# Kernel optimization log

Measured on AMD Instinct MI355X. Metric: run time of the kernel, lower is better.

Reference implementation:

```python
import jax, jax.numpy as jnp
import numpy as np

B, Q, K, D, H = 4, 512, 2048, 256, 64
NEG = -1000000.0


def setup_inputs() -> dict:
    key = jax.random.key(0)
    ks = jax.random.split(key, 7)
    return {
        "queries": jax.random.normal(ks[0], (B, Q, D), dtype=jnp.float32),
        "keys": jax.random.normal(ks[1], (B, K, D), dtype=jnp.float32),
        "values": jax.random.normal(ks[2], (B, K, D), dtype=jnp.float32),
        "valid_lens": jax.random.randint(ks[3], (B,), 0, K).astype(jnp.int64),
        "Wq": jax.random.normal(ks[4], (D, H), dtype=jnp.float32) * 0.05,
        "Wk": jax.random.normal(ks[5], (D, H), dtype=jnp.float32) * 0.05,
        "wv": jax.random.normal(ks[6], (H,), dtype=jnp.float32) * 0.05,
    }


def reference(queries, keys, values, valid_lens, Wq, Wk, wv):
    # project queries/keys to hidden dim
    q = jnp.einsum("bqd,dh->bqh", queries, Wq)  # (B,Q,H)
    k = jnp.einsum("bkd,dh->bkh", keys, Wk)     # (B,K,H)
    # broadcast add + tanh -> (B,Q,K,H), then reduce to scalar score
    features = jnp.tanh(q[:, :, None, :] + k[:, None, :, :])
    scores = jnp.einsum("bqkh,h->bqk", features, wv)  # (B,Q,K)
    # masked softmax over key axis: positions >= valid_len get -1e6
    mask = jnp.arange(scores.shape[-1]) < valid_lens[:, None, None]  # (B,1,K)
    scores = jnp.where(mask, scores, NEG)
    attn = jax.nn.softmax(scores, axis=-1)
    return jnp.einsum("bqk,bkv->bqv", attn, values)
```

## Files before the change

kernel.cpp:

```cpp
#include <hip/hip_runtime.h>
#include <hip/hip_bf16.h>

#define NB 4
#define NQ 512
#define NK 2048
#define ND 256
#define NH 64
#define QT 8
#define KSPLIT 4

#define SCALE_C 2.8853900817779268f
#define L2E     1.4426950408889634f

__device__ __forceinline__ unsigned short f2b(float f) {
    unsigned u = __float_as_uint(f);
    u += 0x7fffu + ((u >> 16) & 1u);
    return (unsigned short)(u >> 16);
}
__device__ __forceinline__ float b2f_lo(unsigned u) { return __uint_as_float(u << 16); }
__device__ __forceinline__ float b2f_hi(unsigned u) { return __uint_as_float(u & 0xffff0000u); }

__device__ __forceinline__ float wred_sum(float v) {
#pragma unroll
    for (int off = 32; off; off >>= 1) v += __shfl_xor(v, off, 64);
    return v;
}

__global__ __launch_bounds__(256) void proj_kernel(
    const float* __restrict__ queries, const float* __restrict__ keys,
    const float* __restrict__ Wq, const float* __restrict__ Wk,
    float* __restrict__ eq, float4* __restrict__ ek4)
{
    __shared__ __align__(16) float in_lds[16][256];
    const int t = threadIdx.x;
    const int row0 = blockIdx.x * 16;
    const bool isQ = row0 < NB * NQ;
    const float* src = isQ ? (queries + (size_t)row0 * ND)
                           : (keys + (size_t)(row0 - NB * NQ) * ND);
    const float* W = isQ ? Wq : Wk;

    const float4* src4 = (const float4*)src;
#pragma unroll
    for (int i = 0; i < 4; ++i) {
        int f4 = t + 256 * i;
        ((float4*)&in_lds[0][0])[f4] = src4[f4];
    }
    __syncthreads();

    const int w = t >> 6, h = t & 63;
    const int r0 = w * 4;
    float a[4] = {0.f, 0.f, 0.f, 0.f};
#pragma unroll 4
    for (int d4 = 0; d4 < 64; ++d4) {
        const float* Wp = W + (size_t)(d4 * 4) * NH + h;
        float w0 = Wp[0], w1 = Wp[NH], w2 = Wp[2 * NH], w3 = Wp[3 * NH];
#pragma unroll
        for (int i = 0; i < 4; ++i) {
            float4 x = ((const float4*)in_lds[r0 + i])[d4];
            a[i] = fmaf(x.x, w0, fmaf(x.y, w1, fmaf(x.z, w2, fmaf(x.w, w3, a[i]))));
        }
    }
    if (isQ) {
#pragma unroll
        for (int i = 0; i < 4; ++i)
            eq[(size_t)(row0 + r0 + i) * NH + h] =
                __builtin_amdgcn_exp2f(a[i] * SCALE_C);
    } else {
        __syncthreads();
        float* out2 = &in_lds[0][0];
#pragma unroll
        for (int i = 0; i < 4; ++i)
            out2[(r0 + i) * 64 + h] = __builtin_amdgcn_exp2f(a[i] * SCALE_C);
        __syncthreads();
        const int row = t >> 4, hb = t & 15;
        float4 v = *(const float4*)&out2[row * 64 + hb * 4];
        int kr = row0 - NB * NQ + row;
        int b = kr >> 11, k = kr & (NK - 1);
        ek4[((size_t)(b * 16 + hb)) * NK + k] = v;
    }
}

__global__ __launch_bounds__(512, 8) void attn_part(
    const float* __restrict__ values, const int* __restrict__ valid_lens,
    const float* __restrict__ wv,
    const float* __restrict__ eq, const float4* __restrict__ ek4,
    float* __restrict__ po, float* __restrict__ pml)
{
    __shared__ __align__(16) float qp_l[QT][NH];
    __shared__ __align__(16) float wv2_l[NH];
    __shared__ float sumwv_l;
    __shared__ __align__(16) float buf[8192];
    __shared__ float red_l[QT][8];

    unsigned short* p_l = (unsigned short*)buf;

    const int t = threadIdx.x;
    const int n = blockIdx.x;
    const int g = n & 255;
    const int sp = n >> 8;
    const int b  = ((g >> 6) + sp) & 3;
    const int qt = g & 63;
    const int q0 = qt * QT;
    const int wid = t >> 6;
    const int dl = (t & 63) * 4;

    if (t < 128) {
        int q = t >> 4, h4 = t & 15;
        ((float4*)qp_l[q])[h4] =
            ((const float4*)(eq + (size_t)(b * NQ + q0 + q) * NH))[h4];
    }
    if (t < 64) {
        float wvv = wv[t];
        wv2_l[t] = -2.0f * wvv;
        float s = wred_sum(wvv);
        if (t == 0) sumwv_l = s;
    }
    int vl = valid_lens[b];
    const int kv = vl < 0 ? 0 : (vl > NK ? NK : vl);
    const int kveff = (kv == 0) ? NK : kv;
    const int step   = ((kveff + 31) & ~31) >> 2;
    const int kvr8   = (kveff + 7) & ~7;
    const int kstart = sp * step;
    int kend = kstart + step; if (kend > kvr8) kend = kvr8;
    const int range8 = (kend > kstart) ? (kend - kstart) : 0;
    __syncthreads();
    const float sumwv = sumwv_l;

    {
        const int kl = t;
        float sum_q[QT];
#pragma unroll
        for (int q = 0; q < QT; ++q) sum_q[q] = 0.f;
        if (kl < range8) {
            const int kg = kstart + kl;
            float e[QT];
            if (kv == 0) {
#pragma unroll
                for (int q = 0; q < QT; ++q) e[q] = 1.0f;
            } else if (kg < kv) {
                float s[QT];
#pragma unroll
                for (int q = 0; q < QT; ++q) s[q] = sumwv;
                const float4* kT4 = ek4 + (size_t)(b * 16) * NK + kg;
#pragma unroll
                for (int gq = 0; gq < 4; ++gq) {
                    float4 kb[4];
#pragma unroll
                    for (int i = 0; i < 4; ++i)
                        kb[i] = kT4[(size_t)(gq * 4 + i) * NK];
#pragma unroll
                    for (int i = 0; i < 4; ++i) {
                        const int h4 = gq * 4 + i;
                        float4 w4 = ((const float4*)wv2_l)[h4];
                        float4 kh = kb[i];
#pragma unroll
                        for (int q = 0; q < QT; ++q) {
                            float4 qh = ((const float4*)qp_l[q])[h4];
                            float d0 = fmaf(qh.x, kh.x, 1.0f);
                            float d1 = fmaf(qh.y, kh.y, 1.0f);
                            float d2 = fmaf(qh.z, kh.z, 1.0f);
                            float d3 = fmaf(qh.w, kh.w, 1.0f);
                            float d01 = d0 * d1;
                            float d23 = d2 * d3;
                            float n01 = w4.x * d1;
                            n01 = fmaf(w4.y, d0, n01);
                            float n23 = w4.z * d3;
                            n23 = fmaf(w4.w, d2, n23);
                            float num = n01 * d23;
                            num = fmaf(n23, d01, num);
                            float r = __builtin_amdgcn_rcpf(d01 * d23);
                            s[q] = fmaf(num, r, s[q]);
                        }
                    }
                }
#pragma unroll
                for (int q = 0; q < QT; ++q) e[q] = __builtin_amdgcn_exp2f(s[q] * L2E);
            } else {
#pragma unroll
                for (int q = 0; q < QT; ++q) e[q] = 0.f;
            }
            unsigned eb[QT];
#pragma unroll
            for (int q = 0; q < QT; ++q) {
                eb[q] = (unsigned)f2b(e[q]);
                sum_q[q] = b2f_lo(eb[q]);
            }
            uint4 u;
            u.x = eb[0] | (eb[1] << 16);
            u.y = eb[2] | (eb[3] << 16);
            u.z = eb[4] | (eb[5] << 16);
            u.w = eb[6] | (eb[7] << 16);
            *(uint4*)&p_l[(size_t)kl * 8] = u;
        }
#pragma unroll
        for (int q = 0; q < QT; ++q) {
            float s = wred_sum(sum_q[q]);
            if ((t & 63) == 0) red_l[q][wid] = s;
        }
    }
    __syncthreads();

    float4 acc[QT];
#pragma unroll
    for (int q = 0; q < QT; ++q) acc[q] = make_float4(0.f, 0.f, 0.f, 0.f);

    const float* Vb = values + ((size_t)b * NK + kstart) * ND;
#pragma unroll 2
    for (int kl = wid; kl < range8; kl += 8) {
        uint4 u = *(const uint4*)&p_l[(size_t)kl * 8];
        float pr0 = b2f_lo(u.x), pr1 = b2f_hi(u.x);
        float pr2 = b2f_lo(u.y), pr3 = b2f_hi(u.y);
        float pr4 = b2f_lo(u.z), pr5 = b2f_hi(u.z);
        float pr6 = b2f_lo(u.w), pr7 = b2f_hi(u.w);
        float4 v = *(const float4*)(Vb + (size_t)kl * ND + dl);
        acc[0].x = fmaf(pr0, v.x, acc[0].x); acc[0].y = fmaf(pr0, v.y, acc[0].y);
        acc[0].z = fmaf(pr0, v.z, acc[0].z); acc[0].w = fmaf(pr0, v.w, acc[0].w);
        acc[1].x = fmaf(pr1, v.x, acc[1].x); acc[1].y = fmaf(pr1, v.y, acc[1].y);
        acc[1].z = fmaf(pr1, v.z, acc[1].z); acc[1].w = fmaf(pr1, v.w, acc[1].w);
        acc[2].x = fmaf(pr2, v.x, acc[2].x); acc[2].y = fmaf(pr2, v.y, acc[2].y);
        acc[2].z = fmaf(pr2, v.z, acc[2].z); acc[2].w = fmaf(pr2, v.w, acc[2].w);
        acc[3].x = fmaf(pr3, v.x, acc[3].x); acc[3].y = fmaf(pr3, v.y, acc[3].y);
        acc[3].z = fmaf(pr3, v.z, acc[3].z); acc[3].w = fmaf(pr3, v.w, acc[3].w);
        acc[4].x = fmaf(pr4, v.x, acc[4].x); acc[4].y = fmaf(pr4, v.y, acc[4].y);
        acc[4].z = fmaf(pr4, v.z, acc[4].z); acc[4].w = fmaf(pr4, v.w, acc[4].w);
        acc[5].x = fmaf(pr5, v.x, acc[5].x); acc[5].y = fmaf(pr5, v.y, acc[5].y);
        acc[5].z = fmaf(pr5, v.z, acc[5].z); acc[5].w = fmaf(pr5, v.w, acc[5].w);
        acc[6].x = fmaf(pr6, v.x, acc[6].x); acc[6].y = fmaf(pr6, v.y, acc[6].y);
        acc[6].z = fmaf(pr6, v.z, acc[6].z); acc[6].w = fmaf(pr6, v.w, acc[6].w);
        acc[7].x = fmaf(pr7, v.x, acc[7].x); acc[7].y = fmaf(pr7, v.y, acc[7].y);
        acc[7].z = fmaf(pr7, v.z, acc[7].z); acc[7].w = fmaf(pr7, v.w, acc[7].w);
    }
    __syncthreads();

    if (wid >= 4) {
        float* s = buf + (size_t)(wid - 4) * 2048;
#pragma unroll
        for (int q = 0; q < QT; ++q) *(float4*)(s + q * 256 + dl) = acc[q];
    }
    __syncthreads();
    if (wid < 4) {
        const float* s = buf + (size_t)wid * 2048;
#pragma unroll
        for (int q = 0; q < QT; ++q) {
            float4 r = *(const float4*)(s + q * 256 + dl);
            acc[q].x += r.x; acc[q].y += r.y; acc[q].z += r.z; acc[q].w += r.w;
        }
    }
    __syncthreads();
    if (wid >= 2 && wid < 4) {
        float* s = buf + (size_t)(wid - 2) * 2048;
#pragma unroll
        for (int q = 0; q < QT; ++q) *(float4*)(s + q * 256 + dl) = acc[q];
    }
    __syncthreads();
    if (wid < 2) {
        const float* s = buf + (size_t)wid * 2048;
#pragma unroll
        for (int q = 0; q < QT; ++q) {
            float4 r = *(const float4*)(s + q * 256 + dl);
            acc[q].x += r.x; acc[q].y += r.y; acc[q].z += r.z; acc[q].w += r.w;
        }
    }
    __syncthreads();
    if (wid == 1) {
#pragma unroll
        for (int q = 0; q < QT; ++q) *(float4*)(buf + q * 256 + dl) = acc[q];
    }
    __syncthreads();
    if (wid == 0) {
#pragma unroll
        for (int q = 0; q < QT; ++q) {
            float4 r = *(const float4*)(buf + q * 256 + dl);
            acc[q].x += r.x; acc[q].y += r.y; acc[q].z += r.z; acc[q].w += r.w;
            const size_t row4 = ((size_t)(b * NQ + q0 + q) * KSPLIT + sp);
            *(float4*)(po + row4 * ND + dl) = acc[q];
        }
        if (t < QT) {
            float l = 0.f;
#pragma unroll
            for (int i = 0; i < 8; ++i) l += red_l[t][i];
            pml[((size_t)(b * NQ + q0 + t) * KSPLIT + sp)] = l;
        }
    }
}

__global__ __launch_bounds__(256) void combine_kernel(
    const float* __restrict__ po, const float* __restrict__ pml,
    float* __restrict__ out)
{
    const int t = threadIdx.x;
    const int row = blockIdx.x * 4 + (t >> 6);
    const int dl = (t & 63) * 4;
    float l = 0.f;
#pragma unroll
    for (int s = 0; s < KSPLIT; ++s) l += pml[row * KSPLIT + s];
    float4 o = make_float4(0.f, 0.f, 0.f, 0.f);
#pragma unroll
    for (int s = 0; s < KSPLIT; ++s) {
        float4 p = *(const float4*)(po + ((size_t)row * KSPLIT + s) * ND + dl);
        o.x += p.x; o.y += p.y; o.z += p.z; o.w += p.w;
    }
    const float inv = 1.0f / l;
    o.x *= inv; o.y *= inv; o.z *= inv; o.w *= inv;
    *(float4*)(out + (size_t)row * ND + dl) = o;
}

extern "C" void kernel_launch(void* const* d_in, const int* in_sizes, int n_in,
                              void* d_out, int out_size, void* d_ws, size_t ws_size,
                              hipStream_t stream) {
    const float* queries   = (const float*)d_in[0];
    const float* keys      = (const float*)d_in[1];
    const float* values    = (const float*)d_in[2];
    const int* valid_lens  = (const int*)d_in[3];
    const float* Wq        = (const float*)d_in[4];
    const float* Wk        = (const float*)d_in[5];
    const float* wv        = (const float*)d_in[6];
    float* out = (float*)d_out;

    float* eq   = (float*)d_ws;
    float4* ek4 = (float4*)(eq + (size_t)NB * NQ * NH);
    float* po   = (float*)(ek4 + (size_t)NB * 16 * NK);
    float* pml  = po + (size_t)NB * NQ * KSPLIT * ND;

    proj_kernel<<<(NB * NQ + NB * NK) / 16, 256, 0, stream>>>(queries, keys, Wq, Wk, eq, ek4);
    attn_part<<<NB * (NQ / QT) * KSPLIT, 512, 0, stream>>>(values, valid_lens, wv, eq, ek4, po, pml);
    combine_kernel<<<NB * NQ / 4, 256, 0, stream>>>(po, pml, out);
}
```

Before: 58.32 us.

## Balance key work across batches with concatenated valid ranges and atomic accumulation

Instead of splitting each batch's valid key range into four fixed chunks, the kernel concatenates the valid key ranges of all batches and splits the total into 16 equal slices per query tile. This evens out work when valid lengths differ across batches. Partial outputs and softmax denominators are accumulated with float atomics into a buffer that the projection kernel now zeroes. The combine step shrinks to a single normalize, at the cost of atomic traffic, extra per-batch tree reductions within a block, and non-deterministic summation order.

```diff
diff --git a/kernel.cpp b/kernel.cpp
--- a/kernel.cpp
+++ b/kernel.cpp
@@ -7,10 +7,13 @@
 #define ND 256
 #define NH 64
 #define QT 8
-#define KSPLIT 4
+#define NSLICE 16
 
 #define SCALE_C 2.8853900817779268f
 #define L2E     1.4426950408889634f
+
+#define PO_FLOATS ((size_t)NB * NQ * ND)
+#define ACC_FLOATS (PO_FLOATS + (size_t)NB * NQ)
 
 __device__ __forceinline__ unsigned short f2b(float f) {
     unsigned u = __float_as_uint(f);
@@ -29,12 +32,23 @@
 __global__ __launch_bounds__(256) void proj_kernel(
     const float* __restrict__ queries, const float* __restrict__ keys,
     const float* __restrict__ Wq, const float* __restrict__ Wk,
-    float* __restrict__ eq, float4* __restrict__ ek4)
+    float* __restrict__ eq, float4* __restrict__ ek4, float* __restrict__ po_acc)
 {
     __shared__ __align__(16) float in_lds[16][256];
     const int t = threadIdx.x;
     const int row0 = blockIdx.x * 16;
     const bool isQ = row0 < NB * NQ;
+
+    {
+        const size_t zb = (size_t)blockIdx.x * 824;
+#pragma unroll
+        for (int i = 0; i < 4; ++i) {
+            int loc = t + i * 256;
+            size_t idx = zb + loc;
+            if (loc < 824 && idx < ACC_FLOATS) po_acc[idx] = 0.f;
+        }
+    }
+
     const float* src = isQ ? (queries + (size_t)row0 * ND)
                            : (keys + (size_t)(row0 - NB * NQ) * ND);
     const float* W = isQ ? Wq : Wk;
@@ -84,105 +98,106 @@
     const float* __restrict__ values, const int* __restrict__ valid_lens,
     const float* __restrict__ wv,
     const float* __restrict__ eq, const float4* __restrict__ ek4,
-    float* __restrict__ po, float* __restrict__ pml)
+    float* __restrict__ po_acc, float* __restrict__ l_acc)
 {
-    __shared__ __align__(16) float qp_l[QT][NH];
-    __shared__ __align__(16) float wv2_l[NH];
-    __shared__ float sumwv_l;
-    __shared__ __align__(16) float buf[8192];
-    __shared__ float red_l[QT][8];
-
-    unsigned short* p_l = (unsigned short*)buf;
+    __shared__ __align__(16) float smem[6468];
+    unsigned short* p_l = (unsigned short*)smem;
+    float* qp_l  = smem + 2048;
+    float* tree  = smem + 2048;
+    float* red_l = smem + 6144;
+    float* wv2_l = smem + 6400;
 
     const int t = threadIdx.x;
-    const int n = blockIdx.x;
-    const int g = n & 255;
-    const int sp = n >> 8;
-    const int b  = ((g >> 6) + sp) & 3;
-    const int qt = g & 63;
+    const int qt = blockIdx.x & 63;
+    const int sp = blockIdx.x >> 6;
     const int q0 = qt * QT;
     const int wid = t >> 6;
     const int dl = (t & 63) * 4;
 
-    if (t < 128) {
-        int q = t >> 4, h4 = t & 15;
-        ((float4*)qp_l[q])[h4] =
+    {
+        int b = t >> 7, q = (t >> 4) & 7, h4 = t & 15;
+        ((float4*)(qp_l + (size_t)(b * 8 + q) * 64))[h4] =
             ((const float4*)(eq + (size_t)(b * NQ + q0 + q) * NH))[h4];
     }
     if (t < 64) {
         float wvv = wv[t];
         wv2_l[t] = -2.0f * wvv;
         float s = wred_sum(wvv);
-        if (t == 0) sumwv_l = s;
-    }
-    int vl = valid_lens[b];
-    const int kv = vl < 0 ? 0 : (vl > NK ? NK : vl);
-    const int kveff = (kv == 0) ? NK : kv;
-    const int step   = ((kveff + 31) & ~31) >> 2;
-    const int kvr8   = (kveff + 7) & ~7;
-    const int kstart = sp * step;
-    int kend = kstart + step; if (kend > kvr8) kend = kvr8;
-    const int range8 = (kend > kstart) ? (kend - kstart) : 0;
+        if (t == 0) smem[6464] = s;
+    }
+    if (t >= 64 && t < 320) red_l[t - 64] = 0.f;
+
+    int kvb[4], C[5];
+    C[0] = 0;
+#pragma unroll
+    for (int b = 0; b < 4; ++b) {
+        int v = valid_lens[b];
+        v = v < 0 ? 0 : (v > NK ? NK : v);
+        kvb[b] = v;
+        int kveff = (v == 0) ? NK : v;
+        C[b + 1] = C[b] + ((kveff + 7) & ~7);
+    }
+    const int T_all = C[4];
+    const int step = ((T_all + 127) & ~127) >> 4;
+    const int cstart = sp * step;
+    int cend = cstart + step; if (cend > T_all) cend = T_all;
     __syncthreads();
-    const float sumwv = sumwv_l;
+    const float sumwv = smem[6464];
 
     {
-        const int kl = t;
+        const int j = cstart + t;
+        const bool act = j < cend;
+        int bb = 3;
+        if (act) bb = (j >= C[1]) + (j >= C[2]) + (j >= C[3]);
+        const int kg = act ? (j - C[bb]) : 0;
+        const int kvB = kvb[bb];
         float sum_q[QT];
 #pragma unroll
         for (int q = 0; q < QT; ++q) sum_q[q] = 0.f;
-        if (kl < range8) {
-            const int kg = kstart + kl;
-            float e[QT];
-            if (kv == 0) {
-#pragma unroll
-                for (int q = 0; q < QT; ++q) e[q] = 1.0f;
-            } else if (kg < kv) {
-                float s[QT];
-#pragma unroll
-                for (int q = 0; q < QT; ++q) s[q] = sumwv;
-                const float4* kT4 = ek4 + (size_t)(b * 16) * NK + kg;
-#pragma unroll
-                for (int gq = 0; gq < 4; ++gq) {
-                    float4 kb[4];
-#pragma unroll
-                    for (int i = 0; i < 4; ++i)
-                        kb[i] = kT4[(size_t)(gq * 4 + i) * NK];
-#pragma unroll
-                    for (int i = 0; i < 4; ++i) {
-                        const int h4 = gq * 4 + i;
-                        float4 w4 = ((const float4*)wv2_l)[h4];
-                        float4 kh = kb[i];
-#pragma unroll
-                        for (int q = 0; q < QT; ++q) {
-                            float4 qh = ((const float4*)qp_l[q])[h4];
-                            float d0 = fmaf(qh.x, kh.x, 1.0f);
-                            float d1 = fmaf(qh.y, kh.y, 1.0f);
-                            float d2 = fmaf(qh.z, kh.z, 1.0f);
-                            float d3 = fmaf(qh.w, kh.w, 1.0f);
-                            float d01 = d0 * d1;
-                            float d23 = d2 * d3;
-                            float n01 = w4.x * d1;
-                            n01 = fmaf(w4.y, d0, n01);
-                            float n23 = w4.z * d3;
-                            n23 = fmaf(w4.w, d2, n23);
-                            float num = n01 * d23;
-                            num = fmaf(n23, d01, num);
-                            float r = __builtin_amdgcn_rcpf(d01 * d23);
-                            s[q] = fmaf(num, r, s[q]);
-                        }
+        if (act) {
+            float s[QT];
+#pragma unroll
+            for (int q = 0; q < QT; ++q) s[q] = sumwv;
+            const float4* kT4 = ek4 + (size_t)(bb * 16) * NK + kg;
+            const float* qb = qp_l + (size_t)bb * 512;
+#pragma unroll
+            for (int gq = 0; gq < 4; ++gq) {
+                float4 kb[4];
+#pragma unroll
+                for (int i = 0; i < 4; ++i) kb[i] = kT4[(size_t)(gq * 4 + i) * NK];
+#pragma unroll
+                for (int i = 0; i < 4; ++i) {
+                    const int h4 = gq * 4 + i;
+                    float4 w4 = ((const float4*)wv2_l)[h4];
+                    float4 kh = kb[i];
+#pragma unroll
+                    for (int q = 0; q < QT; ++q) {
+                        float4 qh = ((const float4*)(qb + q * 64))[h4];
+                        float d0 = fmaf(qh.x, kh.x, 1.0f);
+                        float d1 = fmaf(qh.y, kh.y, 1.0f);
+                        float d2 = fmaf(qh.z, kh.z, 1.0f);
+                        float d3 = fmaf(qh.w, kh.w, 1.0f);
+                        float d01 = d0 * d1;
+                        float d23 = d2 * d3;
+                        float n01 = w4.x * d1;
+                        n01 = fmaf(w4.y, d0, n01);
+                        float n23 = w4.z * d3;
+                        n23 = fmaf(w4.w, d2, n23);
+                        float num = n01 * d23;
+                        num = fmaf(n23, d01, num);
+                        float r = __builtin_amdgcn_rcpf(d01 * d23);
+                        s[q] = fmaf(num, r, s[q]);
                     }
                 }
-#pragma unroll
-                for (int q = 0; q < QT; ++q) e[q] = __builtin_amdgcn_exp2f(s[q] * L2E);
-            } else {
-#pragma unroll
-                for (int q = 0; q < QT; ++q) e[q] = 0.f;
-            }
+            }
+            const bool valid = kg < kvB;
+            const float fill = (kvB == 0) ? 1.0f : 0.0f;
             unsigned eb[QT];
 #pragma unroll
             for (int q = 0; q < QT; ++q) {
-                eb[q] = (unsigned)f2b(e[q]);
+                float ee = __builtin_amdgcn_exp2f(s[q] * L2E);
+                float ev = valid ? ee : fill;
+                eb[q] = (unsigned)f2b(ev);
                 sum_q[q] = b2f_lo(eb[q]);
             }
             uint4 u;
@@ -190,118 +205,139 @@
             u.y = eb[2] | (eb[3] << 16);
             u.z = eb[4] | (eb[5] << 16);
             u.w = eb[6] | (eb[7] << 16);
-            *(uint4*)&p_l[(size_t)kl * 8] = u;
-        }
-#pragma unroll
-        for (int q = 0; q < QT; ++q) {
-            float s = wred_sum(sum_q[q]);
-            if ((t & 63) == 0) red_l[q][wid] = s;
+            *(uint4*)&p_l[(size_t)t * 8] = u;
+        }
+        const int bb0 = __builtin_amdgcn_readfirstlane(bb);
+        const bool uni = __all(bb == bb0);
+        if (uni) {
+#pragma unroll
+            for (int q = 0; q < QT; ++q) {
+                float s = wred_sum(sum_q[q]);
+                if ((t & 63) == 0) red_l[bb0 * 64 + q * 8 + wid] = s;
+            }
+        } else {
+#pragma unroll 1
+            for (int b2 = 0; b2 < 4; ++b2) {
+#pragma unroll
+                for (int q = 0; q < QT; ++q) {
+                    float s = wred_sum(bb == b2 ? sum_q[q] : 0.f);
+                    if ((t & 63) == 0 && s != 0.f) red_l[b2 * 64 + q * 8 + wid] = s;
+                }
+            }
         }
     }
     __syncthreads();
+    if (t < 32) {
+        int b2 = t >> 3, q = t & 7;
+        float l = 0.f;
+#pragma unroll
+        for (int i = 0; i < 8; ++i) l += red_l[b2 * 64 + q * 8 + i];
+        if (l > 0.f) atomicAdd(&l_acc[b2 * NQ + q0 + q], l);
+    }
 
     float4 acc[QT];
-#pragma unroll
-    for (int q = 0; q < QT; ++q) acc[q] = make_float4(0.f, 0.f, 0.f, 0.f);
-
-    const float* Vb = values + ((size_t)b * NK + kstart) * ND;
+#pragma unroll 1
+    for (int b2 = 0; b2 < 4; ++b2) {
+        int g0 = C[b2] > cstart ? C[b2] : cstart;
+        int g1 = C[b2 + 1] < cend ? C[b2 + 1] : cend;
+        if (g0 >= g1) continue;
+        const int s0 = g0 - cstart, s1 = g1 - cstart;
+        const int kg0 = g0 - C[b2];
+#pragma unroll
+        for (int q = 0; q < QT; ++q) acc[q] = make_float4(0.f, 0.f, 0.f, 0.f);
+        const float* Vb = values + ((size_t)b2 * NK + kg0) * ND;
 #pragma unroll 2
-    for (int kl = wid; kl < range8; kl += 8) {
-        uint4 u = *(const uint4*)&p_l[(size_t)kl * 8];
-        float pr0 = b2f_lo(u.x), pr1 = b2f_hi(u.x);
-        float pr2 = b2f_lo(u.y), pr3 = b2f_hi(u.y);
-        float pr4 = b2f_lo(u.z), pr5 = b2f_hi(u.z);
-        float pr6 = b2f_lo(u.w), pr7 = b2f_hi(u.w);
-        float4 v = *(const float4*)(Vb + (size_t)kl * ND + dl);
-        acc[0].x = fmaf(pr0, v.x, acc[0].x); acc[0].y = fmaf(pr0, v.y, acc[0].y);
-        acc[0].z = fmaf(pr0, v.z, acc[0].z); acc[0].w = fmaf(pr0, v.w, acc[0].w);
-        acc[1].x = fmaf(pr1, v.x, acc[1].x); acc[1].y = fmaf(pr1, v.y, acc[1].y);
-        acc[1].z = fmaf(pr1, v.z, acc[1].z); acc[1].w = fmaf(pr1, v.w, acc[1].w);
-        acc[2].x = fmaf(pr2, v.x, acc[2].x); acc[2].y = fmaf(pr2, v.y, acc[2].y);
-        acc[2].z = fmaf(pr2, v.z, acc[2].z); acc[2].w = fmaf(pr2, v.w, acc[2].w);
-        acc[3].x = fmaf(pr3, v.x, acc[3].x); acc[3].y = fmaf(pr3, v.y, acc[3].y);
-        acc[3].z = fmaf(pr3, v.z, acc[3].z); acc[3].w = fmaf(pr3, v.w, acc[3].w);
-        acc[4].x = fmaf(pr4, v.x, acc[4].x); acc[4].y = fmaf(pr4, v.y, acc[4].y);
-        acc[4].z = fmaf(pr4, v.z, acc[4].z); acc[4].w = fmaf(pr4, v.w, acc[4].w);
-        acc[5].x = fmaf(pr5, v.x, acc[5].x); acc[5].y = fmaf(pr5, v.y, acc[5].y);
-        acc[5].z = fmaf(pr5, v.z, acc[5].z); acc[5].w = fmaf(pr5, v.w, acc[5].w);
-        acc[6].x = fmaf(pr6, v.x, acc[6].x); acc[6].y = fmaf(pr6, v.y, acc[6].y);
-        acc[6].z = fmaf(pr6, v.z, acc[6].z); acc[6].w = fmaf(pr6, v.w, acc[6].w);
-        acc[7].x = fmaf(pr7, v.x, acc[7].x); acc[7].y = fmaf(pr7, v.y, acc[7].y);
-        acc[7].z = fmaf(pr7, v.z, acc[7].z); acc[7].w = fmaf(pr7, v.w, acc[7].w);
-    }
-    __syncthreads();
-
-    if (wid >= 4) {
-        float* s = buf + (size_t)(wid - 4) * 2048;
-#pragma unroll
-        for (int q = 0; q < QT; ++q) *(float4*)(s + q * 256 + dl) = acc[q];
-    }
-    __syncthreads();
-    if (wid < 4) {
-        const float* s = buf + (size_t)wid * 2048;
-#pragma unroll
-        for (int q = 0; q < QT; ++q) {
-            float4 r = *(const float4*)(s + q * 256 + dl);
-            acc[q].x += r.x; acc[q].y += r.y; acc[q].z += r.z; acc[q].w += r.w;
-        }
-    }
-    __syncthreads();
-    if (wid >= 2 && wid < 4) {
-        float* s = buf + (size_t)(wid - 2) * 2048;
-#pragma unroll
-        for (int q = 0; q < QT; ++q) *(float4*)(s + q * 256 + dl) = acc[q];
-    }
-    __syncthreads();
-    if (wid < 2) {
-        const float* s = buf + (size_t)wid * 2048;
-#pragma unroll
-        for (int q = 0; q < QT; ++q) {
-            float4 r = *(const float4*)(s + q * 256 + dl);
-            acc[q].x += r.x; acc[q].y += r.y; acc[q].z += r.z; acc[q].w += r.w;
-        }
-    }
-    __syncthreads();
-    if (wid == 1) {
-#pragma unroll
-        for (int q = 0; q < QT; ++q) *(float4*)(buf + q * 256 + dl) = acc[q];
-    }
-    __syncthreads();
-    if (wid == 0) {
-#pragma unroll
-        for (int q = 0; q < QT; ++q) {
-            float4 r = *(const float4*)(buf + q * 256 + dl);
-            acc[q].x += r.x; acc[q].y += r.y; acc[q].z += r.z; acc[q].w += r.w;
-            const size_t row4 = ((size_t)(b * NQ + q0 + q) * KSPLIT + sp);
-            *(float4*)(po + row4 * ND + dl) = acc[q];
-        }
-        if (t < QT) {
-            float l = 0.f;
-#pragma unroll
-            for (int i = 0; i < 8; ++i) l += red_l[t][i];
-            pml[((size_t)(b * NQ + q0 + t) * KSPLIT + sp)] = l;
+        for (int kl = s0 + wid; kl < s1; kl += 8) {
+            uint4 u = *(const uint4*)&p_l[(size_t)kl * 8];
+            float pr0 = b2f_lo(u.x), pr1 = b2f_hi(u.x);
+            float pr2 = b2f_lo(u.y), pr3 = b2f_hi(u.y);
+            float pr4 = b2f_lo(u.z), pr5 = b2f_hi(u.z);
+            float pr6 = b2f_lo(u.w), pr7 = b2f_hi(u.w);
+            float4 v = *(const float4*)(Vb + (size_t)(kl - s0) * ND + dl);
+            acc[0].x = fmaf(pr0, v.x, acc[0].x); acc[0].y = fmaf(pr0, v.y, acc[0].y);
+            acc[0].z = fmaf(pr0, v.z, acc[0].z); acc[0].w = fmaf(pr0, v.w, acc[0].w);
+            acc[1].x = fmaf(pr1, v.x, acc[1].x); acc[1].y = fmaf(pr1, v.y, acc[1].y);
+            acc[1].z = fmaf(pr1, v.z, acc[1].z); acc[1].w = fmaf(pr1, v.w, acc[1].w);
+            acc[2].x = fmaf(pr2, v.x, acc[2].x); acc[2].y = fmaf(pr2, v.y, acc[2].y);
+            acc[2].z = fmaf(pr2, v.z, acc[2].z); acc[2].w = fmaf(pr2, v.w, acc[2].w);
+            acc[3].x = fmaf(pr3, v.x, acc[3].x); acc[3].y = fmaf(pr3, v.y, acc[3].y);
+            acc[3].z = fmaf(pr3, v.z, acc[3].z); acc[3].w = fmaf(pr3, v.w, acc[3].w);
+            acc[4].x = fmaf(pr4, v.x, acc[4].x); acc[4].y = fmaf(pr4, v.y, acc[4].y);
+            acc[4].z = fmaf(pr4, v.z, acc[4].z); acc[4].w = fmaf(pr4, v.w, acc[4].w);
+            acc[5].x = fmaf(pr5, v.x, acc[5].x); acc[5].y = fmaf(pr5, v.y, acc[5].y);
+            acc[5].z = fmaf(pr5, v.z, acc[5].z); acc[5].w = fmaf(pr5, v.w, acc[5].w);
+            acc[6].x = fmaf(pr6, v.x, acc[6].x); acc[6].y = fmaf(pr6, v.y, acc[6].y);
+            acc[6].z = fmaf(pr6, v.z, acc[6].z); acc[6].w = fmaf(pr6, v.w, acc[6].w);
+            acc[7].x = fmaf(pr7, v.x, acc[7].x); acc[7].y = fmaf(pr7, v.y, acc[7].y);
+            acc[7].z = fmaf(pr7, v.z, acc[7].z); acc[7].w = fmaf(pr7, v.w, acc[7].w);
+        }
+        __syncthreads();
+#pragma unroll 1
+        for (int pass = 0; pass < 2; ++pass) {
+            const int qb = pass * 4;
+            if (wid >= 4) {
+                float* sl = tree + (size_t)(wid - 4) * 1024;
+#pragma unroll
+                for (int q = 0; q < 4; ++q) *(float4*)(sl + q * 256 + dl) = acc[qb + q];
+            }
+            __syncthreads();
+            if (wid < 4) {
+                const float* sl = tree + (size_t)wid * 1024;
+#pragma unroll
+                for (int q = 0; q < 4; ++q) {
+                    float4 r = *(const float4*)(sl + q * 256 + dl);
+                    acc[qb+q].x += r.x; acc[qb+q].y += r.y;
+                    acc[qb+q].z += r.z; acc[qb+q].w += r.w;
+                }
+            }
+            __syncthreads();
+            if (wid == 2 || wid == 3) {
+                float* sl = tree + (size_t)(wid - 2) * 1024;
+#pragma unroll
+                for (int q = 0; q < 4; ++q) *(float4*)(sl + q * 256 + dl) = acc[qb + q];
+            }
+            __syncthreads();
+            if (wid < 2) {
+                const float* sl = tree + (size_t)wid * 1024;
+#pragma unroll
+                for (int q = 0; q < 4; ++q) {
+                    float4 r = *(const float4*)(sl + q * 256 + dl);
+                    acc[qb+q].x += r.x; acc[qb+q].y += r.y;
+                    acc[qb+q].z += r.z; acc[qb+q].w += r.w;
+                }
+            }
+            __syncthreads();
+            if (wid == 1) {
+#pragma unroll
+                for (int q = 0; q < 4; ++q) *(float4*)(tree + q * 256 + dl) = acc[qb + q];
+            }
+            __syncthreads();
+            if (wid == 0) {
+#pragma unroll
+                for (int q = 0; q < 4; ++q) {
+                    float4 r = *(const float4*)(tree + q * 256 + dl);
+                    float* base = &po_acc[((size_t)(b2 * NQ + q0 + qb + q)) * ND + dl];
+                    atomicAdd(base + 0, acc[qb+q].x + r.x);
+                    atomicAdd(base + 1, acc[qb+q].y + r.y);
+                    atomicAdd(base + 2, acc[qb+q].z + r.z);
+                    atomicAdd(base + 3, acc[qb+q].w + r.w);
+                }
+            }
+            __syncthreads();
         }
     }
 }
 
 __global__ __launch_bounds__(256) void combine_kernel(
-    const float* __restrict__ po, const float* __restrict__ pml,
+    const float* __restrict__ po_acc, const float* __restrict__ l_acc,
     float* __restrict__ out)
 {
     const int t = threadIdx.x;
     const int row = blockIdx.x * 4 + (t >> 6);
     const int dl = (t & 63) * 4;
-    float l = 0.f;
-#pragma unroll
-    for (int s = 0; s < KSPLIT; ++s) l += pml[row * KSPLIT + s];
-    float4 o = make_float4(0.f, 0.f, 0.f, 0.f);
-#pragma unroll
-    for (int s = 0; s < KSPLIT; ++s) {
-        float4 p = *(const float4*)(po + ((size_t)row * KSPLIT + s) * ND + dl);
-        o.x += p.x; o.y += p.y; o.z += p.z; o.w += p.w;
-    }
-    const float inv = 1.0f / l;
-    o.x *= inv; o.y *= inv; o.z *= inv; o.w *= inv;
+    const float inv = 1.0f / l_acc[row];
+    float4 p = *(const float4*)(po_acc + (size_t)row * ND + dl);
+    float4 o = make_float4(p.x * inv, p.y * inv, p.z * inv, p.w * inv);
     *(float4*)(out + (size_t)row * ND + dl) = o;
 }
 
@@ -317,12 +353,12 @@
     const float* wv        = (const float*)d_in[6];
     float* out = (float*)d_out;
 
-    float* eq   = (float*)d_ws;
-    float4* ek4 = (float4*)(eq + (size_t)NB * NQ * NH);
-    float* po   = (float*)(ek4 + (size_t)NB * 16 * NK);
-    float* pml  = po + (size_t)NB * NQ * KSPLIT * ND;
-
-    proj_kernel<<<(NB * NQ + NB * NK) / 16, 256, 0, stream>>>(queries, keys, Wq, Wk, eq, ek4);
-    attn_part<<<NB * (NQ / QT) * KSPLIT, 512, 0, stream>>>(values, valid_lens, wv, eq, ek4, po, pml);
-    combine_kernel<<<NB * NQ / 4, 256, 0, stream>>>(po, pml, out);
-}
+    float* eq     = (float*)d_ws;
+    float4* ek4   = (float4*)(eq + (size_t)NB * NQ * NH);
+    float* po_acc = (float*)(ek4 + (size_t)NB * 16 * NK);
+    float* l_acc  = po_acc + PO_FLOATS;
+
+    proj_kernel<<<(NB * NQ + NB * NK) / 16, 256, 0, stream>>>(queries, keys, Wq, Wk, eq, ek4, po_acc);
+    attn_part<<<(NQ / QT) * NSLICE, 512, 0, stream>>>(values, valid_lens, wv, eq, ek4, po_acc, l_acc);
+    combine_kernel<<<NB * NQ / 4, 256, 0, stream>>>(po_acc, l_acc, out);
+}
```

Result: slower. 120.6 us (+106.9%).

## Double key split and accumulate partial outputs with atomics instead of combine pass

Applied to the files above, without the earlier changes.

Raises the key-axis split from 4 to 8 so the attention kernel launches twice as many blocks, and replaces the per-split partial output buffers with float atomicAdd into a single accumulator that the projection kernel zeroes. The combine kernel then only scales by the inverse row sum. This aims to raise parallelism on the many-CU GPU and cut the partial-buffer traffic, at the cost of atomic contention, extra per-block overhead for short key ranges, and nondeterministic summation order.

```diff
diff --git a/kernel.cpp b/kernel.cpp
--- a/kernel.cpp
+++ b/kernel.cpp
@@ -7,10 +7,13 @@
 #define ND 256
 #define NH 64
 #define QT 8
-#define KSPLIT 4
+#define KSPLIT 8
 
 #define SCALE_C 2.8853900817779268f
 #define L2E     1.4426950408889634f
+
+#define PO_FLOATS ((size_t)NB * NQ * ND)
+#define ACC_FLOATS (PO_FLOATS + (size_t)NB * NQ)
 
 __device__ __forceinline__ unsigned short f2b(float f) {
     unsigned u = __float_as_uint(f);
@@ -29,12 +32,23 @@
 __global__ __launch_bounds__(256) void proj_kernel(
     const float* __restrict__ queries, const float* __restrict__ keys,
     const float* __restrict__ Wq, const float* __restrict__ Wk,
-    float* __restrict__ eq, float4* __restrict__ ek4)
+    float* __restrict__ eq, float4* __restrict__ ek4, float* __restrict__ po_acc)
 {
     __shared__ __align__(16) float in_lds[16][256];
     const int t = threadIdx.x;
     const int row0 = blockIdx.x * 16;
     const bool isQ = row0 < NB * NQ;
+
+    {
+        const size_t zb = (size_t)blockIdx.x * 824;
+#pragma unroll
+        for (int i = 0; i < 4; ++i) {
+            int loc = t + i * 256;
+            size_t idx = zb + loc;
+            if (loc < 824 && idx < ACC_FLOATS) po_acc[idx] = 0.f;
+        }
+    }
+
     const float* src = isQ ? (queries + (size_t)row0 * ND)
                            : (keys + (size_t)(row0 - NB * NQ) * ND);
     const float* W = isQ ? Wq : Wk;
@@ -84,7 +98,7 @@
     const float* __restrict__ values, const int* __restrict__ valid_lens,
     const float* __restrict__ wv,
     const float* __restrict__ eq, const float4* __restrict__ ek4,
-    float* __restrict__ po, float* __restrict__ pml)
+    float* __restrict__ po_acc, float* __restrict__ l_acc)
 {
     __shared__ __align__(16) float qp_l[QT][NH];
     __shared__ __align__(16) float wv2_l[NH];
@@ -118,7 +132,7 @@
     int vl = valid_lens[b];
     const int kv = vl < 0 ? 0 : (vl > NK ? NK : vl);
     const int kveff = (kv == 0) ? NK : kv;
-    const int step   = ((kveff + 31) & ~31) >> 2;
+    const int step   = ((kveff + 63) & ~63) >> 3;
     const int kvr8   = (kveff + 7) & ~7;
     const int kstart = sp * step;
     int kend = kstart + step; if (kend > kvr8) kend = kvr8;
@@ -272,36 +286,31 @@
         for (int q = 0; q < QT; ++q) {
             float4 r = *(const float4*)(buf + q * 256 + dl);
             acc[q].x += r.x; acc[q].y += r.y; acc[q].z += r.z; acc[q].w += r.w;
-            const size_t row4 = ((size_t)(b * NQ + q0 + q) * KSPLIT + sp);
-            *(float4*)(po + row4 * ND + dl) = acc[q];
+            float* base = &po_acc[((size_t)(b * NQ + q0 + q)) * ND + dl];
+            atomicAdd(base + 0, acc[q].x);
+            atomicAdd(base + 1, acc[q].y);
+            atomicAdd(base + 2, acc[q].z);
+            atomicAdd(base + 3, acc[q].w);
         }
         if (t < QT) {
             float l = 0.f;
 #pragma unroll
             for (int i = 0; i < 8; ++i) l += red_l[t][i];
-            pml[((size_t)(b * NQ + q0 + t) * KSPLIT + sp)] = l;
+            if (l != 0.f) atomicAdd(&l_acc[b * NQ + q0 + t], l);
         }
     }
 }
 
 __global__ __launch_bounds__(256) void combine_kernel(
-    const float* __restrict__ po, const float* __restrict__ pml,
+    const float* __restrict__ po_acc, const float* __restrict__ l_acc,
     float* __restrict__ out)
 {
     const int t = threadIdx.x;
     const int row = blockIdx.x * 4 + (t >> 6);
     const int dl = (t & 63) * 4;
-    float l = 0.f;
-#pragma unroll
-    for (int s = 0; s < KSPLIT; ++s) l += pml[row * KSPLIT + s];
-    float4 o = make_float4(0.f, 0.f, 0.f, 0.f);
-#pragma unroll
-    for (int s = 0; s < KSPLIT; ++s) {
-        float4 p = *(const float4*)(po + ((size_t)row * KSPLIT + s) * ND + dl);
-        o.x += p.x; o.y += p.y; o.z += p.z; o.w += p.w;
-    }
-    const float inv = 1.0f / l;
-    o.x *= inv; o.y *= inv; o.z *= inv; o.w *= inv;
+    const float inv = 1.0f / l_acc[row];
+    float4 p = *(const float4*)(po_acc + (size_t)row * ND + dl);
+    float4 o = make_float4(p.x * inv, p.y * inv, p.z * inv, p.w * inv);
     *(float4*)(out + (size_t)row * ND + dl) = o;
 }
 
@@ -317,12 +326,12 @@
     const float* wv        = (const float*)d_in[6];
     float* out = (float*)d_out;
 
-    float* eq   = (float*)d_ws;
-    float4* ek4 = (float4*)(eq + (size_t)NB * NQ * NH);
-    float* po   = (float*)(ek4 + (size_t)NB * 16 * NK);
-    float* pml  = po + (size_t)NB * NQ * KSPLIT * ND;
-
-    proj_kernel<<<(NB * NQ + NB * NK) / 16, 256, 0, stream>>>(queries, keys, Wq, Wk, eq, ek4);
-    attn_part<<<NB * (NQ / QT) * KSPLIT, 512, 0, stream>>>(values, valid_lens, wv, eq, ek4, po, pml);
-    combine_kernel<<<NB * NQ / 4, 256, 0, stream>>>(po, pml, out);
-}
+    float* eq     = (float*)d_ws;
+    float4* ek4   = (float4*)(eq + (size_t)NB * NQ * NH);
+    float* po_acc = (float*)(ek4 + (size_t)NB * 16 * NK);
+    float* l_acc  = po_acc + PO_FLOATS;
+
+    proj_kernel<<<(NB * NQ + NB * NK) / 16, 256, 0, stream>>>(queries, keys, Wq, Wk, eq, ek4, po_acc);
+    attn_part<<<NB * (NQ / QT) * KSPLIT, 512, 0, stream>>>(values, valid_lens, wv, eq, ek4, po_acc, l_acc);
+    combine_kernel<<<NB * NQ / 4, 256, 0, stream>>>(po_acc, l_acc, out);
+}
```

New measurement: 92.54 us. 1.59x slower.
